# Performance work log

Hardware: AMD Instinct MI355X
Metric: run time of the kernel (lower is better)

## Reference

```python
import jax, jax.numpy as jnp
import numpy as np

KH = KW = 3
SH = SW = 1
PH = PW = 1


def _im2col(x, kh, kw, sh, sw, ph, pw):
    # x: [N, C, H, W] -> cols: [N, C*kh*kw, H_out*W_out], ordering (C, kh, kw)
    N, C, H, W = x.shape
    H_out = (H + 2 * ph - kh) // sh + 1
    W_out = (W + 2 * pw - kw) // sw + 1
    x_pad = jnp.pad(x, ((0, 0), (0, 0), (ph, ph), (pw, pw)))
    # fixed small loop over kernel offsets (kh*kw = 9), strided slices
    patches = [x_pad[:, :, i:i + sh * H_out:sh, j:j + sw * W_out:sw]
               for i in range(kh) for j in range(kw)]  # each [N, C, H_out, W_out]
    cols = jnp.stack(patches, axis=2)  # [N, C, kh*kw, H_out, W_out]
    cols = cols.reshape(N, C * kh * kw, H_out * W_out)
    return cols, H_out, W_out


def setup_inputs() -> dict:
    key = jax.random.key(0)
    k1, k2, k3 = jax.random.split(key, 3)
    x = jax.random.normal(k1, (16, 128, 56, 56), dtype=jnp.float32)
    weight = jax.random.normal(k2, (256, 128, 3, 3), dtype=jnp.float32) * 0.05
    fan_in = 128 * 3 * 3
    bound = 1.0 / fan_in ** 0.5
    bias = jax.random.uniform(k3, (256,), dtype=jnp.float32, minval=-bound, maxval=bound)
    return {"x": x, "weight": weight, "bias": bias}


def reference(x, weight, bias):
    # im2col unfold + (analog) matmul conv; noise_cfg=None -> plain matmul
    cols, H_out, W_out = _im2col(x, KH, KW, SH, SW, PH, PW)  # [N, K, L]
    N = cols.shape[0]
    Cout = weight.shape[0]
    Wmat = weight.reshape(Cout, -1)  # [Cout, K], K = C*kh*kw
    # y[n, l, o] = sum_k cols[n, k, l] * Wmat[o, k]  (AnalogMatMulFn without noise)
    y = jnp.einsum('nkl,ok->nol', cols, Wmat)  # [N, Cout, L]
    y = y.reshape(N, Cout, H_out, W_out)
    y = y + bias[None, :, None, None]
    return y
```

## Files before the change

kernel.cpp:

```cpp
#include <hip/hip_runtime.h>
#include <hip/hip_bf16.h>
#include <stdint.h>


typedef __attribute__((ext_vector_type(8))) short short8;
typedef __attribute__((ext_vector_type(4))) float floatx4;

__device__ static inline void gload_lds16(const void* g, void* l) {
  typedef const __attribute__((address_space(1))) unsigned int* gp_t;
  typedef __attribute__((address_space(3))) unsigned int* lp_t;
  __builtin_amdgcn_global_load_lds((gp_t)(uintptr_t)g, (lp_t)(uint32_t)(uintptr_t)l,
                                   16, 0, 0);
}

__global__ __launch_bounds__(256)
void pre_kernel(const float* __restrict__ x, const float* __restrict__ wsrc,
                __hip_bfloat16* __restrict__ xp, __hip_bfloat16* __restrict__ wt) {
  const int b = blockIdx.x;
  if (b < 16 * 58) {
    const int n = b / 58, hp = b % 58;
    __hip_bfloat16* dst = xp + (size_t)(n * 58 + hp) * 58 * 128;
    if (hp == 0 || hp == 57) {
      const uint4 z = {0, 0, 0, 0};
      uint4* p = (uint4*)dst;
      for (int i = threadIdx.x; i < 928; i += 256) p[i] = z;
      return;
    }
    const int h = hp - 1;
    __shared__ float tile[128][57];
    const float* src = x + (size_t)n * (128 * 3136) + h * 56;
    for (int i = threadIdx.x; i < 128 * 14; i += 256) {
      const int c = i / 14, q = i - c * 14;
      const float4 v = ((const float4*)(src + (size_t)c * 3136))[q];
      tile[c][4 * q + 0] = v.x;
      tile[c][4 * q + 1] = v.y;
      tile[c][4 * q + 2] = v.z;
      tile[c][4 * q + 3] = v.w;
    }
    __syncthreads();
    if (threadIdx.x < 32) {
      const uint4 z = {0, 0, 0, 0};
      const int col = (threadIdx.x >> 4) * 57;
      ((uint4*)(dst + (size_t)col * 128))[threadIdx.x & 15] = z;
    }
    __hip_bfloat16* di = dst + 128;
    for (int i = threadIdx.x; i < 56 * 16; i += 256) {
      const int w = i >> 4, c8 = (i & 15) * 8;
      union { uint4 u; __hip_bfloat16 hh[8]; } pk;
#pragma unroll
      for (int j = 0; j < 8; ++j) pk.hh[j] = __float2bfloat16(tile[c8 + j][w]);
      *(uint4*)(di + (size_t)w * 128 + c8) = pk.u;
    }
  } else {
    const int base = (b - 928) * 256 + threadIdx.x;
    for (int t = base; t < 256 * 9 * 128; t += 36 * 256) {
      const int e = t & 7;
      const int rr = (t >> 3) & 15;
      const int q = (t >> 7) & 3;
      const int ks = (t >> 9) & 1;
      const int ch = (t >> 10) & 1;
      const int t11 = t >> 11;
      const int kq = t11 % 9;
      const int g = t11 / 9;
      const int cout = g * 16 + rr;
      const int c = ch * 64 + ks * 32 + q * 8 + e;
      wt[t] = __float2bfloat16(wsrc[(size_t)(cout * 128 + c) * 9 + kq]);
    }
  }
}

__global__ __launch_bounds__(256, 3)
void conv_gemm_kernel(const __hip_bfloat16* __restrict__ xp,
                      const __hip_bfloat16* __restrict__ wt,
                      const float* __restrict__ bias,
                      float* __restrict__ out) {
  __shared__ __align__(16) char smem[49152];

  const int tid = threadIdx.x;
  const int lane = tid & 63;
  const int wave = tid >> 6;
  const int col = lane & 15;
  const int quad = lane >> 4;

  const int id = blockIdx.x;
  const int xcd = id & 7;
  const int r = id >> 3;
  const int mt_ = r / 98;
  const int nt_ = xcd * 98 + (r - mt_ * 98);
  const int m0 = mt_ * 128;
  const int n0 = nt_ * 64;

  const int nimg0 = n0 / 3136;
  const int rem0 = n0 - nimg0 * 3136;
  const int hh0 = rem0 / 56;
  const int ww0 = rem0 - hh0 * 56;
  const int P0 = (nimg0 * 58 + hh0) * 58 + ww0;
  const char* pbase = (const char*)xp + (size_t)P0 * 256;

#pragma unroll
  for (int i = 0; i < 12; ++i) {
    const int j = i * 256 + tid;
    const int row = j >> 4;
    const int slot = j & 15;
    gload_lds16(pbase + row * 256 + ((slot ^ (row & 7)) << 4),
                smem + i * 4096 + wave * 1024);
  }

  const char* wtb = (const char*)wt;
  const int gbase = (m0 >> 4) + wave * 2;
  const char* pA0 = wtb + (size_t)gbase * 36864 + lane * 16;
  const char* pA1 = pA0 + 36864;

  short8 areg[2][2][2];
#pragma unroll
  for (int ks = 0; ks < 2; ++ks) {
    areg[0][0][ks] = *(const short8*)(pA0 + ks * 1024);
    areg[0][1][ks] = *(const short8*)(pA1 + ks * 1024);
  }

  int rbase[4];
#pragma unroll
  for (int nt = 0; nt < 4; ++nt) {
    const int pix = n0 + nt * 16 + col;
    const int ni = pix / 3136;
    const int re = pix - ni * 3136;
    const int ph = re / 56;
    const int pw = re - ph * 56;
    rbase[nt] = (ni * 58 + ph) * 58 + pw - P0;
  }

  floatx4 acc[2][4];
#pragma unroll
  for (int a = 0; a < 2; ++a)
#pragma unroll
    for (int c = 0; c < 4; ++c) acc[a][c] = (floatx4)0.f;

  __syncthreads();

#pragma unroll
  for (int s = 0; s < 18; ++s) {
    const int cur = s & 1, nxt = cur ^ 1;
    if (s < 17) {
      const int s1 = s + 1;
      const int ofs = (s1 >> 1) * 4096 + (s1 & 1) * 2048;
#pragma unroll
      for (int ks = 0; ks < 2; ++ks) {
        areg[nxt][0][ks] = *(const short8*)(pA0 + ofs + ks * 1024);
        areg[nxt][1][ks] = *(const short8*)(pA1 + ofs + ks * 1024);
      }
    }
    const int kq = s >> 1, ch = s & 1;
    const int kh = kq / 3;
    const int tofs = kh * 58 + (kq - kh * 3);
    short8 bf[4][2];
#pragma unroll
    for (int nt = 0; nt < 4; ++nt) {
      const int rowB = rbase[nt] + tofs;
#pragma unroll
      for (int ks = 0; ks < 2; ++ks) {
        const int cB = ch * 8 + ks * 4 + quad;
        const int pos = cB ^ (rowB & 7);
        bf[nt][ks] = *(const short8*)(smem + rowB * 256 + (pos << 4));
      }
    }
#pragma unroll
    for (int ks = 0; ks < 2; ++ks)
#pragma unroll
      for (int mt = 0; mt < 2; ++mt)
#pragma unroll
        for (int nt = 0; nt < 4; ++nt)
          acc[mt][nt] = __builtin_amdgcn_mfma_f32_16x16x32_bf16(
              areg[cur][mt][ks], bf[nt][ks], acc[mt][nt], 0, 0, 0);
  }

  const int rb = quad * 4;
#pragma unroll
  for (int nt = 0; nt < 4; ++nt) {
    const int pix = n0 + nt * 16 + col;
    const int nimg = pix / 3136;
    const int rem = pix - nimg * 3136;
    float* op = out + (size_t)nimg * (256 * 3136) + rem;
#pragma unroll
    for (int mt = 0; mt < 2; ++mt) {
      const int mb = m0 + wave * 32 + mt * 16 + rb;
#pragma unroll
      for (int rr = 0; rr < 4; ++rr) {
        op[(size_t)(mb + rr) * 3136] = acc[mt][nt][rr] + bias[mb + rr];
      }
    }
  }
}

__global__ __launch_bounds__(256)
void direct_conv_kernel(const float* __restrict__ x, const float* __restrict__ wgt,
                        const float* __restrict__ bias, float* __restrict__ out) {
  const long t = (long)blockIdx.x * 256 + threadIdx.x;
  if (t >= 16L * 256 * 3136) return;
  const int w = t % 56;
  const int h = (t / 56) % 56;
  const int o = (t / 3136) % 256;
  const int n = t / (256L * 3136);
  float s = bias[o];
  for (int c = 0; c < 128; ++c)
    for (int kh = 0; kh < 3; ++kh) {
      const int hh = h + kh - 1;
      if (hh < 0 || hh >= 56) continue;
      for (int kw = 0; kw < 3; ++kw) {
        const int ww = w + kw - 1;
        if (ww < 0 || ww >= 56) continue;
        s += x[((size_t)(n * 128 + c) * 56 + hh) * 56 + ww] *
             wgt[((size_t)(o * 128 + c) * 3 + kh) * 3 + kw];
      }
    }
  out[t] = s;
}

extern "C" void kernel_launch(void* const* d_in, const int* in_sizes, int n_in,
                              void* d_out, int out_size, void* d_ws, size_t ws_size,
                              hipStream_t stream) {
  const float* x = (const float*)d_in[0];
  const float* w = (const float*)d_in[1];
  const float* b = (const float*)d_in[2];
  float* out = (float*)d_out;

  const size_t xp_bytes = (size_t)16 * 58 * 58 * 128 * 2;
  const size_t wt_bytes = (size_t)256 * 9 * 128 * 2;

  if (ws_size >= xp_bytes + wt_bytes) {
    __hip_bfloat16* xp = (__hip_bfloat16*)d_ws;
    __hip_bfloat16* wt = (__hip_bfloat16*)((char*)d_ws + xp_bytes);
    hipLaunchKernelGGL(pre_kernel, dim3(16 * 58 + 36), dim3(256), 0, stream,
                       x, w, xp, wt);
    hipLaunchKernelGGL(conv_gemm_kernel, dim3(1568), dim3(256), 0, stream,
                       xp, wt, b, out);
  } else {
    const long total = 16L * 256 * 3136;
    hipLaunchKernelGGL(direct_conv_kernel, dim3((unsigned)((total + 255) / 256)),
                       dim3(256), 0, stream, x, w, b, out);
  }
}
```

Before: 125.8 us.

## Cover all 256 output channels per block, halving grid and reusing B tile

Each block now computes all 256 output channels for its 64-pixel tile, with each wave handling 64 channels (4 M sub-tiles), instead of splitting M into two 128-channel blocks. This halves the grid and avoids loading and staging the same input halo tile into LDS twice. The A-fragment register double-buffering prefetch is dropped in favour of loading weights inside each step. The trade-offs are a doubled accumulator footprint, which raises register pressure and may hurt occupancy under launch bounds of 3 blocks per SM, and exposed global-load latency for the weights. With 784 blocks, there is also less parallelism for hiding that latency.

```diff
diff --git a/kernel.cpp b/kernel.cpp
--- a/kernel.cpp
+++ b/kernel.cpp
@@ -85,9 +85,7 @@
   const int id = blockIdx.x;
   const int xcd = id & 7;
   const int r = id >> 3;
-  const int mt_ = r / 98;
-  const int nt_ = xcd * 98 + (r - mt_ * 98);
-  const int m0 = mt_ * 128;
+  const int nt_ = xcd * 98 + r;
   const int n0 = nt_ * 64;
 
   const int nimg0 = n0 / 3136;
@@ -107,16 +105,7 @@
   }
 
   const char* wtb = (const char*)wt;
-  const int gbase = (m0 >> 4) + wave * 2;
-  const char* pA0 = wtb + (size_t)gbase * 36864 + lane * 16;
-  const char* pA1 = pA0 + 36864;
-
-  short8 areg[2][2][2];
-#pragma unroll
-  for (int ks = 0; ks < 2; ++ks) {
-    areg[0][0][ks] = *(const short8*)(pA0 + ks * 1024);
-    areg[0][1][ks] = *(const short8*)(pA1 + ks * 1024);
-  }
+  const char* pA = wtb + (size_t)(wave * 4) * 36864 + lane * 16;
 
   int rbase[4];
 #pragma unroll
@@ -129,9 +118,9 @@
     rbase[nt] = (ni * 58 + ph) * 58 + pw - P0;
   }
 
-  floatx4 acc[2][4];
-#pragma unroll
-  for (int a = 0; a < 2; ++a)
+  floatx4 acc[4][4];
+#pragma unroll
+  for (int a = 0; a < 4; ++a)
 #pragma unroll
     for (int c = 0; c < 4; ++c) acc[a][c] = (floatx4)0.f;
 
@@ -139,19 +128,18 @@
 
 #pragma unroll
   for (int s = 0; s < 18; ++s) {
-    const int cur = s & 1, nxt = cur ^ 1;
-    if (s < 17) {
-      const int s1 = s + 1;
-      const int ofs = (s1 >> 1) * 4096 + (s1 & 1) * 2048;
-#pragma unroll
-      for (int ks = 0; ks < 2; ++ks) {
-        areg[nxt][0][ks] = *(const short8*)(pA0 + ofs + ks * 1024);
-        areg[nxt][1][ks] = *(const short8*)(pA1 + ofs + ks * 1024);
-      }
-    }
     const int kq = s >> 1, ch = s & 1;
     const int kh = kq / 3;
     const int tofs = kh * 58 + (kq - kh * 3);
+    const int aofs = kq * 4096 + ch * 2048;
+
+    short8 af[4][2];
+#pragma unroll
+    for (int mt = 0; mt < 4; ++mt)
+#pragma unroll
+      for (int ks = 0; ks < 2; ++ks)
+        af[mt][ks] = *(const short8*)(pA + mt * 36864 + aofs + ks * 1024);
+
     short8 bf[4][2];
 #pragma unroll
     for (int nt = 0; nt < 4; ++nt) {
@@ -163,14 +151,15 @@
         bf[nt][ks] = *(const short8*)(smem + rowB * 256 + (pos << 4));
       }
     }
+
 #pragma unroll
     for (int ks = 0; ks < 2; ++ks)
 #pragma unroll
-      for (int mt = 0; mt < 2; ++mt)
+      for (int mt = 0; mt < 4; ++mt)
 #pragma unroll
         for (int nt = 0; nt < 4; ++nt)
           acc[mt][nt] = __builtin_amdgcn_mfma_f32_16x16x32_bf16(
-              areg[cur][mt][ks], bf[nt][ks], acc[mt][nt], 0, 0, 0);
+              af[mt][ks], bf[nt][ks], acc[mt][nt], 0, 0, 0);
   }
 
   const int rb = quad * 4;
@@ -181,8 +170,8 @@
     const int rem = pix - nimg * 3136;
     float* op = out + (size_t)nimg * (256 * 3136) + rem;
 #pragma unroll
-    for (int mt = 0; mt < 2; ++mt) {
-      const int mb = m0 + wave * 32 + mt * 16 + rb;
+    for (int mt = 0; mt < 4; ++mt) {
+      const int mb = wave * 64 + mt * 16 + rb;
 #pragma unroll
       for (int rr = 0; rr < 4; ++rr) {
         op[(size_t)(mb + rr) * 3136] = acc[mt][nt][rr] + bias[mb + rr];
@@ -231,7 +220,7 @@
     __hip_bfloat16* wt = (__hip_bfloat16*)((char*)d_ws + xp_bytes);
     hipLaunchKernelGGL(pre_kernel, dim3(16 * 58 + 36), dim3(256), 0, stream,
                        x, w, xp, wt);
-    hipLaunchKernelGGL(conv_gemm_kernel, dim3(1568), dim3(256), 0, stream,
+    hipLaunchKernelGGL(conv_gemm_kernel, dim3(784), dim3(256), 0, stream,
                        xp, wt, b, out);
   } else {
     const long total = 16L * 256 * 3136;
```

Result: slower. 128.8 us (+2.4%).
